# Performance work log

Hardware: AMD Instinct MI355X
Metric: run time of the kernel (lower is better)

## Reference

```python
import jax, jax.numpy as jnp
import numpy as np

B, SQ, SK, DIMG, DTXT, D, H = 512, 49, 50, 2048, 768, 512, 4
DH = D // H
LN_EPS = 1e-5


def _proj_head(x, W1, b1, W2, b2, g, be):
    # Linear -> GELU -> Linear -> residual -> LayerNorm (dropout = eval/no-op)
    p = x @ W1 + b1
    h = jax.nn.gelu(p, approximate=False) @ W2 + b2 + p
    mu = h.mean(-1, keepdims=True)
    var = ((h - mu) ** 2).mean(-1, keepdims=True)
    return g * (h - mu) * jax.lax.rsqrt(var + LN_EPS) + be


def setup_inputs() -> dict:
    key = jax.random.key(0)
    ks = jax.random.split(key, 12)
    s = 0.02
    inp = {
        'image_features': jax.random.normal(ks[0], (B, DIMG, SQ), jnp.float32),
        'text_embeddings': jax.random.normal(ks[1], (B, SK, DTXT), jnp.float32),
        # image projection head (2048 -> 512)
        'Wi1': jax.random.normal(ks[2], (DIMG, D), jnp.float32) * s,
        'bi1': jnp.zeros((D,), jnp.float32),
        'Wi2': jax.random.normal(ks[3], (D, D), jnp.float32) * s,
        'bi2': jnp.zeros((D,), jnp.float32),
        'gi': jnp.ones((D,), jnp.float32),
        'bei': jnp.zeros((D,), jnp.float32),
        # text projection head (768 -> 512)
        'Wt1': jax.random.normal(ks[4], (DTXT, D), jnp.float32) * s,
        'bt1': jnp.zeros((D,), jnp.float32),
        'Wt2': jax.random.normal(ks[5], (D, D), jnp.float32) * s,
        'bt2': jnp.zeros((D,), jnp.float32),
        'gt': jnp.ones((D,), jnp.float32),
        'bet': jnp.zeros((D,), jnp.float32),
        # multihead cross-attention (embed_dim=512, 4 heads)
        'Wq': jax.random.normal(ks[6], (D, D), jnp.float32) * s,
        'bq': jnp.zeros((D,), jnp.float32),
        'Wk': jax.random.normal(ks[7], (D, D), jnp.float32) * s,
        'bk': jnp.zeros((D,), jnp.float32),
        'Wv': jax.random.normal(ks[8], (D, D), jnp.float32) * s,
        'bv': jnp.zeros((D,), jnp.float32),
        'Wo': jax.random.normal(ks[9], (D, D), jnp.float32) * s,
        'bo': jnp.zeros((D,), jnp.float32),
    }
    return inp


def reference(image_features, text_embeddings,
              Wi1, bi1, Wi2, bi2, gi, bei,
              Wt1, bt1, Wt2, bt2, gt, bet,
              Wq, bq, Wk, bk, Wv, bv, Wo, bo):
    img = jnp.transpose(image_features, (0, 2, 1))          # [B,SQ,2048]
    pi = _proj_head(img, Wi1, bi1, Wi2, bi2, gi, bei)        # [B,SQ,D]
    pt = _proj_head(text_embeddings, Wt1, bt1, Wt2, bt2, gt, bet)  # [B,SK,D]

    # cross attention: query = image tokens, key/value = text tokens
    q = (pi @ Wq + bq).reshape(B, SQ, H, DH)
    k = (pt @ Wk + bk).reshape(B, SK, H, DH)
    v = (pt @ Wv + bv).reshape(B, SK, H, DH)
    scores = jnp.einsum('bqhd,bkhd->bhqk', q, k) * (1.0 / np.sqrt(DH))
    a = jax.nn.softmax(scores, axis=-1)                      # [B,H,SQ,SK]
    o = jnp.einsum('bhqk,bkhd->bqhd', a, v).reshape(B, SQ, D)
    attn_output = o @ Wo + bo                                # [B,SQ,D]
    attn_weights = a.mean(axis=1)                            # torch MHA averages heads

    avg_attn = attn_output.mean(axis=1)                      # AdaptiveAvgPool1d(1) over SQ
    cls = pt[:, 0, :]                                        # [B,D]

    # cosine-similarity matrix: one normalize + matmul replaces B*B kernel launches
    n1 = avg_attn / jnp.linalg.norm(avg_attn, axis=-1, keepdims=True)
    n2 = cls / jnp.linalg.norm(cls, axis=-1, keepdims=True)
    score = n1 @ n2.T                                        # [B,B]
    return (score, attn_output, attn_weights, pi, pt)
```

## Files before the change

### kernel.cpp

```cpp
#include <hip/hip_runtime.h>
#include <math.h>

#define B_    512
#define SQ_   49
#define SK_   50
#define DIMG_ 2048
#define DTXT_ 768
#define D_    512
#define H_    4
#define DH_   128

#define SCORE_OFF 0
#define AO_OFF    262144
#define AW_OFF    13107200
#define PI_OFF    14361600
#define PT_OFF    27206656

typedef unsigned short bfbits;
typedef __attribute__((ext_vector_type(8))) short short8;
typedef __attribute__((ext_vector_type(4))) float floatx4;

static __device__ __forceinline__ bfbits f2bf(float f) {
    union { float f; unsigned u; } a; a.f = f;
    return (bfbits)((a.u + 0x7fffu + ((a.u >> 16) & 1u)) >> 16);
}
static __device__ __forceinline__ float bf2f(bfbits b) {
    union { unsigned u; float f; } a; a.u = ((unsigned)b) << 16;
    return a.f;
}
static __device__ __forceinline__ float gelu_exact(float x) {
    return 0.5f * x * (1.0f + erff(x * 0.70710678118654752f));
}

__global__ __launch_bounds__(256) void wcast_t(
    const float* __restrict__ W, bfbits* __restrict__ Wt, int K, int N)
{
    __shared__ float t[32][33];
    const int k0 = blockIdx.x * 32, n0 = blockIdx.y * 32;
    const int tx = threadIdx.x & 31, ty = threadIdx.x >> 5;
    #pragma unroll
    for (int i = 0; i < 32; i += 8)
        t[ty + i][tx] = W[(size_t)(k0 + ty + i) * N + n0 + tx];
    __syncthreads();
    #pragma unroll
    for (int i = 0; i < 32; i += 8)
        Wt[(size_t)(n0 + ty + i) * K + k0 + tx] = f2bf(t[tx][ty + i]);
}

__global__ __launch_bounds__(256) void img_t(
    const float* __restrict__ img, bfbits* __restrict__ A)
{
    __shared__ float t[64][50];
    const int b = blockIdx.y, k0 = blockIdx.x * 64;
    const float* src = img + (size_t)b * (DIMG_ * SQ_) + (size_t)k0 * SQ_;
    for (int e = threadIdx.x; e < 64 * 49; e += 256) {
        int kl = e / 49, s = e - kl * 49;
        t[kl][s] = src[kl * 49 + s];
    }
    __syncthreads();
    bfbits* dst = A + (size_t)b * SQ_ * DIMG_ + k0;
    for (int e = threadIdx.x; e < 49 * 64; e += 256) {
        int s = e >> 6, kl = e & 63;
        dst[(size_t)s * DIMG_ + kl] = f2bf(t[kl][s]);
    }
}

__global__ __launch_bounds__(256) void cast4(
    const float* __restrict__ x, bfbits* __restrict__ y, int n4)
{
    int i = blockIdx.x * 256 + threadIdx.x;
    if (i < n4) {
        float4 v = ((const float4*)x)[i];
        ushort4 u;
        u.x = f2bf(v.x); u.y = f2bf(v.y); u.z = f2bf(v.z); u.w = f2bf(v.w);
        ((ushort4*)y)[i] = u;
    }
}

template<bool RES, bool GELU, bool WF32, bool WBF>
__global__ __launch_bounds__(256) void gemm_bf16(
    const bfbits* __restrict__ A, const bfbits* __restrict__ Bt,
    const float* __restrict__ bias, const float* res,
    float* Cf, bfbits* __restrict__ Cb, int M, int K)
{
    constexpr int N = 512;
    __shared__ __attribute__((aligned(16))) bfbits As[3][128 * 32];
    __shared__ __attribute__((aligned(16))) bfbits Bs[3][128 * 32];
    const int tid  = threadIdx.x;
    const int wave = tid >> 6, lane = tid & 63;

    const int nwg = gridDim.x;
    const int o = blockIdx.x;
    const int qch = nwg >> 3;
    const int lg = (o & 7) * qch + (o >> 3);
    const int m0 = (lg >> 2) * 128, n0 = (lg & 3) * 128;

    const int wm = (wave >> 1) * 64, wn = (wave & 1) * 64;
    const int lr = lane & 15, quad = lane >> 4;

    floatx4 acc[4][4];
    #pragma unroll
    for (int i = 0; i < 4; ++i)
        #pragma unroll
        for (int j = 0; j < 4; ++j) acc[i][j] = 0.0f;

    const int srow = lane >> 2;
    const int skof = (lane & 3) * 8;

    auto stage = [&](int buf, int t) {
        const int k0 = t * 32;
        #pragma unroll
        for (int i = 0; i < 2; ++i) {
            const int c = wave * 2 + i;
            const int row = c * 16 + srow;
            const bfbits* ga = A + (size_t)(m0 + row) * K + k0 + skof;
            const bfbits* gb = Bt + (size_t)(n0 + row) * K + k0 + skof;
            __builtin_amdgcn_global_load_lds(
                (const __attribute__((address_space(1))) void*)ga,
                (__attribute__((address_space(3))) void*)(&As[buf][c * 512]), 16, 0, 0);
            __builtin_amdgcn_global_load_lds(
                (const __attribute__((address_space(1))) void*)gb,
                (__attribute__((address_space(3))) void*)(&Bs[buf][c * 512]), 16, 0, 0);
        }
    };

    const int nt = K >> 5;
    stage(0, 0);
    stage(1, 1);
    stage(2, 2);

    int cur = 0;
    for (int t = 0; t < nt; ++t) {
        const int left = nt - 1 - t;
        if (left >= 2)      asm volatile("s_waitcnt vmcnt(8)" ::: "memory");
        else if (left == 1) asm volatile("s_waitcnt vmcnt(4)" ::: "memory");
        else                asm volatile("s_waitcnt vmcnt(0)" ::: "memory");
        __builtin_amdgcn_s_barrier();

        short8 af[4], bfv[4];
        #pragma unroll
        for (int i = 0; i < 4; ++i) {
            af[i]  = *(const short8*)(&As[cur][(wm + i * 16 + lr) * 32 + quad * 8]);
            bfv[i] = *(const short8*)(&Bs[cur][(wn + i * 16 + lr) * 32 + quad * 8]);
        }
        asm volatile("s_waitcnt lgkmcnt(0)" ::: "memory");
        __builtin_amdgcn_s_barrier();

        if (t + 3 < nt) stage(cur, t + 3);

        __builtin_amdgcn_s_setprio(1);
        #pragma unroll
        for (int i = 0; i < 4; ++i)
            #pragma unroll
            for (int j = 0; j < 4; ++j)
                acc[i][j] = __builtin_amdgcn_mfma_f32_16x16x32_bf16(
                    af[i], bfv[j], acc[i][j], 0, 0, 0);
        __builtin_amdgcn_s_setprio(0);

        cur = (cur == 2) ? 0 : cur + 1;
    }

    #pragma unroll
    for (int i = 0; i < 4; ++i) {
        #pragma unroll
        for (int j = 0; j < 4; ++j) {
            const int gc = n0 + wn + j * 16 + lr;
            const float bv = bias[gc];
            #pragma unroll
            for (int r = 0; r < 4; ++r) {
                const int gm = m0 + wm + i * 16 + quad * 4 + r;
                float v = acc[i][j][r] + bv;
                if (RES) v += res[(size_t)gm * N + gc];
                if (WF32) Cf[(size_t)gm * N + gc] = v;
                if (GELU) Cb[(size_t)gm * N + gc] = f2bf(gelu_exact(v));
                else if (WBF) Cb[(size_t)gm * N + gc] = f2bf(v);
            }
        }
    }
}

__global__ __launch_bounds__(256) void ln2_kernel(
    const float* __restrict__ h, const float* __restrict__ g,
    const float* __restrict__ be, float* __restrict__ outf,
    bfbits* __restrict__ outb)
{
    __shared__ float red[256];
    const int row = blockIdx.x;
    const int tid = threadIdx.x;
    float v0 = h[(size_t)row * D_ + tid];
    float v1 = h[(size_t)row * D_ + 256 + tid];
    red[tid] = v0 + v1;
    __syncthreads();
    for (int s = 128; s > 0; s >>= 1) {
        if (tid < s) red[tid] += red[tid + s];
        __syncthreads();
    }
    float mu = red[0] * (1.0f / 512.0f);
    __syncthreads();
    float d0 = v0 - mu, d1 = v1 - mu;
    red[tid] = d0 * d0 + d1 * d1;
    __syncthreads();
    for (int s = 128; s > 0; s >>= 1) {
        if (tid < s) red[tid] += red[tid + s];
        __syncthreads();
    }
    float var = red[0] * (1.0f / 512.0f);
    float sc = rsqrtf(var + 1e-5f);
    float o0 = g[tid] * d0 * sc + be[tid];
    float o1 = g[256 + tid] * d1 * sc + be[256 + tid];
    outf[(size_t)row * D_ + tid]       = o0;
    outf[(size_t)row * D_ + 256 + tid] = o1;
    outb[(size_t)row * D_ + tid]       = f2bf(o0);
    outb[(size_t)row * D_ + 256 + tid] = f2bf(o1);
}

__global__ __launch_bounds__(256) void attn_kernel(
    const bfbits* __restrict__ q, const bfbits* __restrict__ k,
    const bfbits* __restrict__ v, bfbits* __restrict__ o,
    float* __restrict__ aw)
{
    constexpr int ROWF = 69;
    __shared__ float sc[H_][SQ_ * ROWF];
    const int b = blockIdx.x;
    const int tid = threadIdx.x;
    const int h = tid >> 6, lane = tid & 63;
    const int lr = lane & 15, g = lane >> 4;

    const bfbits* kb = k + ((size_t)b * SK_) * D_ + h * DH_;
    const bfbits* qb = q + ((size_t)b * SQ_) * D_ + h * DH_;

    floatx4 acc[4][4];
    #pragma unroll
    for (int mi = 0; mi < 4; ++mi)
        #pragma unroll
        for (int ni = 0; ni < 4; ++ni) acc[mi][ni] = 0.0f;

    #pragma unroll
    for (int ks = 0; ks < 4; ++ks) {
        short8 afr[4], bfr[4];
        #pragma unroll
        for (int mi = 0; mi < 4; ++mi)
            afr[mi] = *(const short8*)(kb + (size_t)(mi * 16 + lr) * D_ + ks * 32 + g * 8);
        #pragma unroll
        for (int ni = 0; ni < 4; ++ni)
            bfr[ni] = *(const short8*)(qb + (size_t)(ni * 16 + lr) * D_ + ks * 32 + g * 8);
        #pragma unroll
        for (int mi = 0; mi < 4; ++mi)
            #pragma unroll
            for (int ni = 0; ni < 4; ++ni)
                acc[mi][ni] = __builtin_amdgcn_mfma_f32_16x16x32_bf16(
                    afr[mi], bfr[ni], acc[mi][ni], 0, 0, 0);
    }

    const float scale = 0.08838834764831845f;
    #pragma unroll
    for (int ni = 0; ni < 4; ++ni) {
        const int qi = ni * 16 + lr;
        float mx = -1e30f;
        #pragma unroll
        for (int mi = 0; mi < 4; ++mi)
            #pragma unroll
            for (int r = 0; r < 4; ++r) {
                const int ki = mi * 16 + g * 4 + r;
                float s = (ki < SK_) ? acc[mi][ni][r] * scale : -1e30f;
                acc[mi][ni][r] = s;
                mx = fmaxf(mx, s);
            }
        mx = fmaxf(mx, __shfl_xor(mx, 16));
        mx = fmaxf(mx, __shfl_xor(mx, 32));
        float sum = 0.f;
        #pragma unroll
        for (int mi = 0; mi < 4; ++mi)
            #pragma unroll
            for (int r = 0; r < 4; ++r) {
                float ev = __expf(acc[mi][ni][r] - mx);
                acc[mi][ni][r] = ev;
                sum += ev;
            }
        sum += __shfl_xor(sum, 16);
        sum += __shfl_xor(sum, 32);
        const float inv = 1.0f / sum;
        if (qi < SQ_) {
            #pragma unroll
            for (int mi = 0; mi < 4; ++mi) {
                float4 w;
                w.x = acc[mi][ni][0] * inv;
                w.y = acc[mi][ni][1] * inv;
                w.z = acc[mi][ni][2] * inv;
                w.w = acc[mi][ni][3] * inv;
                *(float4*)&sc[h][qi * ROWF + mi * 16 + g * 4] = w;
            }
        }
    }
    __syncthreads();

    for (int e = tid; e < SQ_ * SK_; e += 256) {
        int qi = e / SK_, ki = e - qi * SK_;
        const int off = qi * ROWF + ki;
        aw[(size_t)b * (SQ_ * SK_) + e] =
            0.25f * (sc[0][off] + sc[1][off] + sc[2][off] + sc[3][off]);
    }

    const bfbits* vb = v + ((size_t)b * SK_) * D_ + h * DH_;
    bfbits* ob = o + ((size_t)b * SQ_) * D_ + h * DH_;
    for (int e = lane; e < SQ_ * 16; e += 64) {
        const int qi = e >> 4, dc = e & 15;
        const float* sr = &sc[h][qi * ROWF];
        float s[8] = {0.f, 0.f, 0.f, 0.f, 0.f, 0.f, 0.f, 0.f};
        for (int ki = 0; ki < SK_; ++ki) {
            const float a = sr[ki];
            short8 u = *(const short8*)(vb + (size_t)ki * D_ + dc * 8);
            #pragma unroll
            for (int j = 0; j < 8; ++j)
                s[j] = fmaf(a, bf2f((bfbits)u[j]), s[j]);
        }
        short8 ov;
        #pragma unroll
        for (int j = 0; j < 8; ++j) ov[j] = (short)f2bf(s[j]);
        *(short8*)(ob + (size_t)qi * D_ + dc * 8) = ov;
    }
}

__global__ __launch_bounds__(256) void norm_kernel(
    const float* __restrict__ ao, const float* __restrict__ pt,
    float* __restrict__ n1, float* __restrict__ n2)
{
    __shared__ float red[256];
    const int b = blockIdx.x, tid = threadIdx.x;
    float s0 = 0.f, s1 = 0.f;
    for (int s = 0; s < SQ_; ++s) {
        s0 += ao[((size_t)(b * SQ_ + s)) * D_ + tid];
        s1 += ao[((size_t)(b * SQ_ + s)) * D_ + 256 + tid];
    }
    s0 *= (1.0f / 49.0f);
    s1 *= (1.0f / 49.0f);
    red[tid] = s0 * s0 + s1 * s1;
    __syncthreads();
    for (int st = 128; st > 0; st >>= 1) {
        if (tid < st) red[tid] += red[tid + st];
        __syncthreads();
    }
    float inv = rsqrtf(red[0]);
    __syncthreads();
    n1[(size_t)b * D_ + tid] = s0 * inv;
    n1[(size_t)b * D_ + 256 + tid] = s1 * inv;

    float c0 = pt[((size_t)(b * SK_)) * D_ + tid];
    float c1 = pt[((size_t)(b * SK_)) * D_ + 256 + tid];
    red[tid] = c0 * c0 + c1 * c1;
    __syncthreads();
    for (int st = 128; st > 0; st >>= 1) {
        if (tid < st) red[tid] += red[tid + st];
        __syncthreads();
    }
    float inv2 = rsqrtf(red[0]);
    n2[(size_t)b * D_ + tid] = c0 * inv2;
    n2[(size_t)b * D_ + 256 + tid] = c1 * inv2;
}

__global__ __launch_bounds__(256) void score_gemm(
    const float* __restrict__ A, const float* __restrict__ Bm,
    float* __restrict__ C)
{
    const int BM = 64, BN = 64, BK = 16, Kt = 512, Nt = 512;
    __shared__ float As[BK][BM + 1];
    __shared__ float Bs[BK][BN + 1];
    const int tid = threadIdx.x;
    const int m0 = blockIdx.y * BM, n0 = blockIdx.x * BN;
    const int tc = tid & 15, tr = tid >> 4;
    float acc[4][4] = {};
    for (int k0 = 0; k0 < Kt; k0 += BK) {
        #pragma unroll
        for (int i = 0; i < 4; ++i) {
            int idx = tid + i * 256;
            int m = idx >> 4, kk = idx & 15;
            As[kk][m] = A[(size_t)(m0 + m) * Kt + k0 + kk];
            Bs[kk][m] = Bm[(size_t)(n0 + m) * Kt + k0 + kk];
        }
        __syncthreads();
        #pragma unroll
        for (int kk = 0; kk < BK; ++kk) {
            float a4[4], b4[4];
            #pragma unroll
            for (int i = 0; i < 4; ++i) a4[i] = As[kk][tr * 4 + i];
            #pragma unroll
            for (int j = 0; j < 4; ++j) b4[j] = Bs[kk][tc * 4 + j];
            #pragma unroll
            for (int i = 0; i < 4; ++i)
                #pragma unroll
                for (int j = 0; j < 4; ++j)
                    acc[i][j] = fmaf(a4[i], b4[j], acc[i][j]);
        }
        __syncthreads();
    }
    #pragma unroll
    for (int i = 0; i < 4; ++i)
        #pragma unroll
        for (int j = 0; j < 4; ++j)
            C[(size_t)(m0 + tr * 4 + i) * Nt + n0 + tc * 4 + j] = acc[i][j];
}

extern "C" void kernel_launch(void* const* d_in, const int* in_sizes, int n_in,
                              void* d_out, int out_size, void* d_ws, size_t ws_size,
                              hipStream_t stream)
{
    const float* img = (const float*)d_in[0];
    const float* txt = (const float*)d_in[1];
    const float* Wi1 = (const float*)d_in[2];  const float* bi1 = (const float*)d_in[3];
    const float* Wi2 = (const float*)d_in[4];  const float* bi2 = (const float*)d_in[5];
    const float* gi  = (const float*)d_in[6];  const float* bei = (const float*)d_in[7];
    const float* Wt1 = (const float*)d_in[8];  const float* bt1 = (const float*)d_in[9];
    const float* Wt2 = (const float*)d_in[10]; const float* bt2 = (const float*)d_in[11];
    const float* gt  = (const float*)d_in[12]; const float* bet = (const float*)d_in[13];
    const float* Wq  = (const float*)d_in[14]; const float* bq  = (const float*)d_in[15];
    const float* Wk  = (const float*)d_in[16]; const float* bk  = (const float*)d_in[17];
    const float* Wv  = (const float*)d_in[18]; const float* bv  = (const float*)d_in[19];
    const float* Wo  = (const float*)d_in[20]; const float* bo  = (const float*)d_in[21];
    float* out = (float*)d_out;

    bfbits* Wi1T = (bfbits*)d_ws;
    bfbits* Wi2T = Wi1T + 1048576;
    bfbits* Wt1T = Wi2T + 262144;
    bfbits* Wt2T = Wt1T + 393216;
    bfbits* WqT  = Wt2T + 262144;
    bfbits* WkT  = WqT  + 262144;
    bfbits* WvT  = WkT  + 262144;
    bfbits* WoT  = WvT  + 262144;
    bfbits* R1   = WoT  + 262144;
    bfbits* Aimg = R1;
    bfbits* Atxt = R1;
    bfbits* Qbf  = R1 + 20000000;
    bfbits* Kbf  = R1 + 33200000;
    float*  R2   = (float*)(R1 + 51380224);
    bfbits* Vbf  = (bfbits*)R2;
    bfbits* R3   = (bfbits*)(R2 + 13107200);
    bfbits* Obf  = R3;
    bfbits* PiBf = R3 + 13107200;
    bfbits* PtBf = PiBf + 12845056;
    float*  n1   = (float*)(PtBf + 13107200);
    float*  n2   = n1 + 262144;

    const int MI = B_ * SQ_;
    const int MT = B_ * SK_;
    dim3 blk(256);

    wcast_t<<<dim3(DIMG_ / 32, D_ / 32), blk, 0, stream>>>(Wi1, Wi1T, DIMG_, D_);
    wcast_t<<<dim3(D_ / 32, D_ / 32),    blk, 0, stream>>>(Wi2, Wi2T, D_, D_);
    wcast_t<<<dim3(DTXT_ / 32, D_ / 32), blk, 0, stream>>>(Wt1, Wt1T, DTXT_, D_);
    wcast_t<<<dim3(D_ / 32, D_ / 32),    blk, 0, stream>>>(Wt2, Wt2T, D_, D_);
    wcast_t<<<dim3(D_ / 32, D_ / 32),    blk, 0, stream>>>(Wq, WqT, D_, D_);
    wcast_t<<<dim3(D_ / 32, D_ / 32),    blk, 0, stream>>>(Wk, WkT, D_, D_);
    wcast_t<<<dim3(D_ / 32, D_ / 32),    blk, 0, stream>>>(Wv, WvT, D_, D_);
    wcast_t<<<dim3(D_ / 32, D_ / 32),    blk, 0, stream>>>(Wo, WoT, D_, D_);

    img_t<<<dim3(DIMG_ / 64, B_), blk, 0, stream>>>(img, Aimg);
    gemm_bf16<false, true, true, true><<<dim3(4 * (MI / 128)), blk, 0, stream>>>(
        Aimg, Wi1T, bi1, nullptr, R2, R3, MI, DIMG_);
    gemm_bf16<true, false, true, false><<<dim3(4 * (MI / 128)), blk, 0, stream>>>(
        R3, Wi2T, bi2, R2, R2, nullptr, MI, D_);
    ln2_kernel<<<dim3(MI), blk, 0, stream>>>(R2, gi, bei, out + PI_OFF, PiBf);

    cast4<<<dim3((MT * DTXT_ / 4 + 255) / 256), blk, 0, stream>>>(txt, Atxt, MT * DTXT_ / 4);
    gemm_bf16<false, true, true, true><<<dim3(4 * (MT / 128)), blk, 0, stream>>>(
        Atxt, Wt1T, bt1, nullptr, R2, R3, MT, DTXT_);
    gemm_bf16<true, false, true, false><<<dim3(4 * (MT / 128)), blk, 0, stream>>>(
        R3, Wt2T, bt2, R2, R2, nullptr, MT, D_);
    ln2_kernel<<<dim3(MT), blk, 0, stream>>>(R2, gt, bet, out + PT_OFF, PtBf);

    gemm_bf16<false, false, false, true><<<dim3(4 * (MI / 128)), blk, 0, stream>>>(
        PiBf, WqT, bq, nullptr, nullptr, Qbf, MI, D_);
    gemm_bf16<false, false, false, true><<<dim3(4 * (MT / 128)), blk, 0, stream>>>(
        PtBf, WkT, bk, nullptr, nullptr, Kbf, MT, D_);
    gemm_bf16<false, false, false, true><<<dim3(4 * (MT / 128)), blk, 0, stream>>>(
        PtBf, WvT, bv, nullptr, nullptr, Vbf, MT, D_);

    attn_kernel<<<dim3(B_), blk, 0, stream>>>(Qbf, Kbf, Vbf, Obf, out + AW_OFF);

    gemm_bf16<false, false, true, false><<<dim3(4 * (MI / 128)), blk, 0, stream>>>(
        Obf, WoT, bo, nullptr, out + AO_OFF, nullptr, MI, D_);

    norm_kernel<<<dim3(B_), blk, 0, stream>>>(out + AO_OFF, out + PT_OFF, n1, n2);
    score_gemm<<<dim3(8, 8), blk, 0, stream>>>(n1, n2, out + SCORE_OFF);
}
```

Measured before the change: 1.041 ms.

## Enlarge GEMM tile to 256x128 with 512 threads, double buffering, wave-per-row LayerNorm

The GEMM now uses 512-thread blocks computing 256x128 output tiles, with eight waves each still owning a 64x64 subtile. The LDS pipeline drops from triple to double buffering to keep shared memory in check. Each wave issues three async loads per stage to cover the larger A tile. The goal is more reuse of the B tile and fewer workgroups. LayerNorm is rewritten so one wave handles one row, using vectorized loads and shuffle reductions instead of a shared-memory tree with many barriers. The trade-off is a shallower prefetch depth and a coarser grid, which could leave some CUs idle on the tail.

```diff
diff --git a/kernel.cpp b/kernel.cpp
--- a/kernel.cpp
+++ b/kernel.cpp
@@ -78,14 +78,14 @@
 }
 
 template<bool RES, bool GELU, bool WF32, bool WBF>
-__global__ __launch_bounds__(256) void gemm_bf16(
+__global__ __launch_bounds__(512, 4) void gemm_bf16(
     const bfbits* __restrict__ A, const bfbits* __restrict__ Bt,
     const float* __restrict__ bias, const float* res,
     float* Cf, bfbits* __restrict__ Cb, int M, int K)
 {
     constexpr int N = 512;
-    __shared__ __attribute__((aligned(16))) bfbits As[3][128 * 32];
-    __shared__ __attribute__((aligned(16))) bfbits Bs[3][128 * 32];
+    __shared__ __attribute__((aligned(16))) bfbits As[2][256 * 32];
+    __shared__ __attribute__((aligned(16))) bfbits Bs[2][128 * 32];
     const int tid  = threadIdx.x;
     const int wave = tid >> 6, lane = tid & 63;
 
@@ -93,7 +93,7 @@
     const int o = blockIdx.x;
     const int qch = nwg >> 3;
     const int lg = (o & 7) * qch + (o >> 3);
-    const int m0 = (lg >> 2) * 128, n0 = (lg & 3) * 128;
+    const int m0 = (lg >> 2) * 256, n0 = (lg & 3) * 128;
 
     const int wm = (wave >> 1) * 64, wn = (wave & 1) * 64;
     const int lr = lane & 15, quad = lane >> 4;
@@ -110,31 +110,30 @@
     auto stage = [&](int buf, int t) {
         const int k0 = t * 32;
         #pragma unroll
-        for (int i = 0; i < 2; ++i) {
-            const int c = wave * 2 + i;
-            const int row = c * 16 + srow;
-            const bfbits* ga = A + (size_t)(m0 + row) * K + k0 + skof;
-            const bfbits* gb = Bt + (size_t)(n0 + row) * K + k0 + skof;
-            __builtin_amdgcn_global_load_lds(
-                (const __attribute__((address_space(1))) void*)ga,
-                (__attribute__((address_space(3))) void*)(&As[buf][c * 512]), 16, 0, 0);
-            __builtin_amdgcn_global_load_lds(
-                (const __attribute__((address_space(1))) void*)gb,
-                (__attribute__((address_space(3))) void*)(&Bs[buf][c * 512]), 16, 0, 0);
+        for (int i = 0; i < 3; ++i) {
+            const int c = wave * 3 + i;
+            if (c < 16) {
+                const bfbits* ga = A + (size_t)(m0 + c * 16 + srow) * K + k0 + skof;
+                __builtin_amdgcn_global_load_lds(
+                    (const __attribute__((address_space(1))) void*)ga,
+                    (__attribute__((address_space(3))) void*)(&As[buf][c * 512]), 16, 0, 0);
+            } else {
+                const bfbits* gb = Bt + (size_t)(n0 + (c - 16) * 16 + srow) * K + k0 + skof;
+                __builtin_amdgcn_global_load_lds(
+                    (const __attribute__((address_space(1))) void*)gb,
+                    (__attribute__((address_space(3))) void*)(&Bs[buf][(c - 16) * 512]), 16, 0, 0);
+            }
         }
     };
 
     const int nt = K >> 5;
     stage(0, 0);
     stage(1, 1);
-    stage(2, 2);
 
     int cur = 0;
     for (int t = 0; t < nt; ++t) {
-        const int left = nt - 1 - t;
-        if (left >= 2)      asm volatile("s_waitcnt vmcnt(8)" ::: "memory");
-        else if (left == 1) asm volatile("s_waitcnt vmcnt(4)" ::: "memory");
-        else                asm volatile("s_waitcnt vmcnt(0)" ::: "memory");
+        if (t + 1 < nt) asm volatile("s_waitcnt vmcnt(3)" ::: "memory");
+        else            asm volatile("s_waitcnt vmcnt(0)" ::: "memory");
         __builtin_amdgcn_s_barrier();
 
         short8 af[4], bfv[4];
@@ -146,7 +145,7 @@
         asm volatile("s_waitcnt lgkmcnt(0)" ::: "memory");
         __builtin_amdgcn_s_barrier();
 
-        if (t + 3 < nt) stage(cur, t + 3);
+        if (t + 2 < nt) stage(cur, t + 2);
 
         __builtin_amdgcn_s_setprio(1);
         #pragma unroll
@@ -157,7 +156,7 @@
                     af[i], bfv[j], acc[i][j], 0, 0, 0);
         __builtin_amdgcn_s_setprio(0);
 
-        cur = (cur == 2) ? 0 : cur + 1;
+        cur ^= 1;
     }
 
     #pragma unroll
@@ -184,34 +183,43 @@
     const float* __restrict__ be, float* __restrict__ outf,
     bfbits* __restrict__ outb)
 {
-    __shared__ float red[256];
-    const int row = blockIdx.x;
-    const int tid = threadIdx.x;
-    float v0 = h[(size_t)row * D_ + tid];
-    float v1 = h[(size_t)row * D_ + 256 + tid];
-    red[tid] = v0 + v1;
-    __syncthreads();
-    for (int s = 128; s > 0; s >>= 1) {
-        if (tid < s) red[tid] += red[tid + s];
-        __syncthreads();
-    }
-    float mu = red[0] * (1.0f / 512.0f);
-    __syncthreads();
-    float d0 = v0 - mu, d1 = v1 - mu;
-    red[tid] = d0 * d0 + d1 * d1;
-    __syncthreads();
-    for (int s = 128; s > 0; s >>= 1) {
-        if (tid < s) red[tid] += red[tid + s];
-        __syncthreads();
-    }
-    float var = red[0] * (1.0f / 512.0f);
-    float sc = rsqrtf(var + 1e-5f);
-    float o0 = g[tid] * d0 * sc + be[tid];
-    float o1 = g[256 + tid] * d1 * sc + be[256 + tid];
-    outf[(size_t)row * D_ + tid]       = o0;
-    outf[(size_t)row * D_ + 256 + tid] = o1;
-    outb[(size_t)row * D_ + tid]       = f2bf(o0);
-    outb[(size_t)row * D_ + 256 + tid] = f2bf(o1);
+    const int wave = threadIdx.x >> 6, lane = threadIdx.x & 63;
+    const size_t row = (size_t)blockIdx.x * 4 + wave;
+    const float* hr = h + row * D_ + lane * 8;
+    float4 a = *(const float4*)hr;
+    float4 b = *(const float4*)(hr + 4);
+    float v[8] = {a.x, a.y, a.z, a.w, b.x, b.y, b.z, b.w};
+
+    float s = v[0] + v[1] + v[2] + v[3] + v[4] + v[5] + v[6] + v[7];
+    #pragma unroll
+    for (int d = 1; d < 64; d <<= 1) s += __shfl_xor(s, d);
+    const float mu = s * (1.0f / 512.0f);
+
+    float vs = 0.f;
+    #pragma unroll
+    for (int i = 0; i < 8; ++i) { v[i] -= mu; vs += v[i] * v[i]; }
+    #pragma unroll
+    for (int d = 1; d < 64; d <<= 1) vs += __shfl_xor(vs, d);
+    const float sc = rsqrtf(vs * (1.0f / 512.0f) + 1e-5f);
+
+    const float* gp = g + lane * 8;
+    const float* bp = be + lane * 8;
+    float4 g0 = *(const float4*)gp, g1 = *(const float4*)(gp + 4);
+    float4 b0 = *(const float4*)bp, b1 = *(const float4*)(bp + 4);
+    float gg[8] = {g0.x, g0.y, g0.z, g0.w, g1.x, g1.y, g1.z, g1.w};
+    float bb[8] = {b0.x, b0.y, b0.z, b0.w, b1.x, b1.y, b1.z, b1.w};
+
+    float o[8];
+    short8 ob;
+    #pragma unroll
+    for (int i = 0; i < 8; ++i) {
+        o[i] = gg[i] * v[i] * sc + bb[i];
+        ob[i] = (short)f2bf(o[i]);
+    }
+    float* of = outf + row * D_ + lane * 8;
+    *(float4*)of       = make_float4(o[0], o[1], o[2], o[3]);
+    *(float4*)(of + 4) = make_float4(o[4], o[5], o[6], o[7]);
+    *(short8*)(outb + row * D_ + lane * 8) = ob;
 }
 
 __global__ __launch_bounds__(256) void attn_kernel(
@@ -443,6 +451,7 @@
     const int MI = B_ * SQ_;
     const int MT = B_ * SK_;
     dim3 blk(256);
+    dim3 blk512(512);
 
     wcast_t<<<dim3(DIMG_ / 32, D_ / 32), blk, 0, stream>>>(Wi1, Wi1T, DIMG_, D_);
     wcast_t<<<dim3(D_ / 32, D_ / 32),    blk, 0, stream>>>(Wi2, Wi2T, D_, D_);
@@ -454,29 +463,29 @@
     wcast_t<<<dim3(D_ / 32, D_ / 32),    blk, 0, stream>>>(Wo, WoT, D_, D_);
 
     img_t<<<dim3(DIMG_ / 64, B_), blk, 0, stream>>>(img, Aimg);
-    gemm_bf16<false, true, true, true><<<dim3(4 * (MI / 128)), blk, 0, stream>>>(
+    gemm_bf16<false, true, true, true><<<dim3(4 * (MI / 256)), blk512, 0, stream>>>(
         Aimg, Wi1T, bi1, nullptr, R2, R3, MI, DIMG_);
-    gemm_bf16<true, false, true, false><<<dim3(4 * (MI / 128)), blk, 0, stream>>>(
+    gemm_bf16<true, false, true, false><<<dim3(4 * (MI / 256)), blk512, 0, stream>>>(
         R3, Wi2T, bi2, R2, R2, nullptr, MI, D_);
-    ln2_kernel<<<dim3(MI), blk, 0, stream>>>(R2, gi, bei, out + PI_OFF, PiBf);
+    ln2_kernel<<<dim3(MI / 4), blk, 0, stream>>>(R2, gi, bei, out + PI_OFF, PiBf);
 
     cast4<<<dim3((MT * DTXT_ / 4 + 255) / 256), blk, 0, stream>>>(txt, Atxt, MT * DTXT_ / 4);
-    gemm_bf16<false, true, true, true><<<dim3(4 * (MT / 128)), blk, 0, stream>>>(
+    gemm_bf16<false, true, true, true><<<dim3(4 * (MT / 256)), blk512, 0, stream>>>(
         Atxt, Wt1T, bt1, nullptr, R2, R3, MT, DTXT_);
-    gemm_bf16<true, false, true, false><<<dim3(4 * (MT / 128)), blk, 0, stream>>>(
+    gemm_bf16<true, false, true, false><<<dim3(4 * (MT / 256)), blk512, 0, stream>>>(
         R3, Wt2T, bt2, R2, R2, nullptr, MT, D_);
-    ln2_kernel<<<dim3(MT), blk, 0, stream>>>(R2, gt, bet, out + PT_OFF, PtBf);
-
-    gemm_bf16<false, false, false, true><<<dim3(4 * (MI / 128)), blk, 0, stream>>>(
+    ln2_kernel<<<dim3(MT / 4), blk, 0, stream>>>(R2, gt, bet, out + PT_OFF, PtBf);
+
+    gemm_bf16<false, false, false, true><<<dim3(4 * (MI / 256)), blk512, 0, stream>>>(
         PiBf, WqT, bq, nullptr, nullptr, Qbf, MI, D_);
-    gemm_bf16<false, false, false, true><<<dim3(4 * (MT / 128)), blk, 0, stream>>>(
+    gemm_bf16<false, false, false, true><<<dim3(4 * (MT / 256)), blk512, 0, stream>>>(
         PtBf, WkT, bk, nullptr, nullptr, Kbf, MT, D_);
-    gemm_bf16<false, false, false, true><<<dim3(4 * (MT / 128)), blk, 0, stream>>>(
+    gemm_bf16<false, false, false, true><<<dim3(4 * (MT / 256)), blk512, 0, stream>>>(
         PtBf, WvT, bv, nullptr, nullptr, Vbf, MT, D_);
 
     attn_kernel<<<dim3(B_), blk, 0, stream>>>(Qbf, Kbf, Vbf, Obf, out + AW_OFF);
 
-    gemm_bf16<false, false, true, false><<<dim3(4 * (MI / 128)), blk, 0, stream>>>(
+    gemm_bf16<false, false, true, false><<<dim3(4 * (MI / 256)), blk512, 0, stream>>>(
         Obf, WoT, bo, nullptr, out + AO_OFF, nullptr, MI, D_);
 
     norm_kernel<<<dim3(B_), blk, 0, stream>>>(out + AO_OFF, out + PT_OFF, n1, n2);
```

After: 940.8 us. 1.11x faster.
